# Optimization experiments

Hardware: AMD Instinct MI355X
Metric: run time of the kernel (lower is better)

## Reference

```python
import jax, jax.numpy as jnp
import numpy as np

B, S, H, F, E, K = 2, 2048, 1024, 4096, 8, 2
NH = H // 128  # heads of dim 128, per SimpleMoEBlock.__init__
DH = H // NH


def _layernorm(x, g, b, eps=1e-5):
    m = x.mean(-1, keepdims=True)
    v = ((x - m) ** 2).mean(-1, keepdims=True)
    return (x - m) / jnp.sqrt(v + eps) * g + b


def _forward(x, ln_attn_g, ln_attn_b, ln_mlp_g, ln_mlp_b,
             in_proj_w, in_proj_b, out_proj_w, out_proj_b,
             router_w, fc1_w, fc1_b, fc2_w, fc2_b):
    # --- self attention (nn.MultiheadAttention, batch_first, no mask) ---
    xa = _layernorm(x, ln_attn_g, ln_attn_b)                    # [B,S,H]
    qkv = xa @ in_proj_w.T + in_proj_b                          # [B,S,3H]
    q, k, v = jnp.split(qkv, 3, axis=-1)
    def heads(t):
        return t.reshape(B, S, NH, DH).transpose(0, 2, 1, 3)    # [B,NH,S,DH]
    q, k, v = heads(q), heads(k), heads(v)
    scores = jnp.einsum('bhqd,bhkd->bhqk', q, k) / jnp.sqrt(jnp.asarray(DH, x.dtype))
    attn = jnp.einsum('bhqk,bhkd->bhqd', jax.nn.softmax(scores, axis=-1), v)
    attn = attn.transpose(0, 2, 1, 3).reshape(B, S, H)
    attn = attn @ out_proj_w.T + out_proj_b
    h = x + attn                                                # residual

    # --- MoE feed-forward ---
    y = _layernorm(h, ln_mlp_g, ln_mlp_b).reshape(B * S, H)     # flat tokens [T,H]
    logits = y @ router_w.T                                     # [T,E]
    probs = jax.nn.softmax(logits, axis=-1)
    top_scores, top_idx = jax.lax.top_k(probs, K)               # [T,K]
    # per-token per-expert combine weight; 0 for unrouted tokens -> identical
    # math to torch's index_select/index_add dispatch
    w = (jax.nn.one_hot(top_idx, E, dtype=y.dtype) * top_scores[..., None]).sum(axis=1)  # [T,E]

    combined = jnp.zeros_like(y)
    for e in range(E):  # fixed small expert count
        he = jax.nn.silu(y @ fc1_w[e].T + fc1_b[e])             # [T,F]
        oe = he @ fc2_w[e].T + fc2_b[e]                         # [T,H]
        combined = combined + oe * w[:, e:e + 1]
    return h + combined.reshape(B, S, H)


def setup_inputs() -> dict:
    key = jax.random.key(0)
    ks = jax.random.split(key, 8)
    s = 0.02
    return {
        'x': jax.random.normal(ks[0], (B, S, H), jnp.float32),
        'ln_attn_g': jnp.ones((H,), jnp.float32),
        'ln_attn_b': jnp.zeros((H,), jnp.float32),
        'ln_mlp_g': jnp.ones((H,), jnp.float32),
        'ln_mlp_b': jnp.zeros((H,), jnp.float32),
        'in_proj_w': jax.random.normal(ks[1], (3 * H, H), jnp.float32) * s,
        'in_proj_b': jnp.zeros((3 * H,), jnp.float32),
        'out_proj_w': jax.random.normal(ks[2], (H, H), jnp.float32) * s,
        'out_proj_b': jnp.zeros((H,), jnp.float32),
        'router_w': jax.random.normal(ks[3], (E, H), jnp.float32) * s,
        'fc1_w': jax.random.normal(ks[4], (E, F, H), jnp.float32) * s,
        'fc1_b': jnp.zeros((E, F), jnp.float32),
        'fc2_w': jax.random.normal(ks[5], (E, H, F), jnp.float32) * s,
        'fc2_b': jnp.zeros((E, H), jnp.float32),
    }


def reference(x, ln_attn_g, ln_attn_b, ln_mlp_g, ln_mlp_b,
              in_proj_w, in_proj_b, out_proj_w, out_proj_b,
              router_w, fc1_w, fc1_b, fc2_w, fc2_b):
    return _forward(x, ln_attn_g, ln_attn_b, ln_mlp_g, ln_mlp_b,
                    in_proj_w, in_proj_b, out_proj_w, out_proj_b,
                    router_w, fc1_w, fc1_b, fc2_w, fc2_b)
```

## Files before the change

### kernel.cpp

```cpp
#include <hip/hip_runtime.h>

#define T_TOK 4096
#define S_SEQ 2048
#define H_DIM 1024
#define H3    3072
#define NHEAD 8
#define DHEAD 128
#define F_DIM 4096
#define NEXP  8
#define MAX_RB 72
#define NSLOT 9216

typedef __bf16 bf16x8 __attribute__((ext_vector_type(8)));
typedef float  f32x4  __attribute__((ext_vector_type(4)));
typedef __attribute__((address_space(1))) const unsigned int* gas1_t;
typedef __attribute__((address_space(3))) unsigned int* las3_t;

__device__ __forceinline__ unsigned short f2bf(float f){
  unsigned int u = __builtin_bit_cast(unsigned int, f);
  u += 0x7fffu + ((u>>16)&1u);
  return (unsigned short)(u>>16);
}
__device__ __forceinline__ float bf2f(unsigned short h){
  unsigned int u = ((unsigned int)h)<<16;
  return __builtin_bit_cast(float, u);
}
__device__ __forceinline__ f32x4 MF(bf16x8 a, bf16x8 b, f32x4 c){
  return __builtin_amdgcn_mfma_f32_16x16x32_bf16(a,b,c,0,0,0);
}
__device__ __forceinline__ void gload16(const void* g, void* l){
  __builtin_amdgcn_global_load_lds((gas1_t)g, (las3_t)l, 16, 0, 0);
}
__device__ __forceinline__ float blockReduceSum(float v){
  __shared__ float sh_red[4];
  #pragma unroll
  for(int o=32;o>0;o>>=1) v += __shfl_down(v,o,64);
  int w = threadIdx.x>>6;
  if((threadIdx.x&63)==0) sh_red[w]=v;
  __syncthreads();
  float tot = sh_red[0]+sh_red[1]+sh_red[2]+sh_red[3];
  __syncthreads();
  return tot;
}

__global__ __launch_bounds__(256) void k_ln_split(const float* __restrict__ x,
    const float* __restrict__ g, const float* __restrict__ bta,
    unsigned short* __restrict__ hi, unsigned short* __restrict__ lo){
  int t = blockIdx.x, tid = threadIdx.x;
  float4 v = reinterpret_cast<const float4*>(x + (size_t)t*H_DIM)[tid];
  float mean = blockReduceSum(v.x+v.y+v.z+v.w) * (1.0f/H_DIM);
  float d0=v.x-mean,d1=v.y-mean,d2=v.z-mean,d3=v.w-mean;
  float var = blockReduceSum(d0*d0+d1*d1+d2*d2+d3*d3) * (1.0f/H_DIM);
  float rstd = rsqrtf(var + 1e-5f);
  float4 gv = reinterpret_cast<const float4*>(g)[tid];
  float4 bv = reinterpret_cast<const float4*>(bta)[tid];
  float o0=d0*rstd*gv.x+bv.x, o1=d1*rstd*gv.y+bv.y, o2=d2*rstd*gv.z+bv.z, o3=d3*rstd*gv.w+bv.w;
  size_t base = (size_t)t*H_DIM + tid*4;
  unsigned short h0=f2bf(o0),h1=f2bf(o1),h2=f2bf(o2),h3=f2bf(o3);
  *reinterpret_cast<ushort4*>(hi+base) = make_ushort4(h0,h1,h2,h3);
  *reinterpret_cast<ushort4*>(lo+base) = make_ushort4(
      f2bf(o0-bf2f(h0)), f2bf(o1-bf2f(h1)), f2bf(o2-bf2f(h2)), f2bf(o3-bf2f(h3)));
}

__global__ __launch_bounds__(256) void k_wsplit(const float* __restrict__ w,
    unsigned short* __restrict__ hi, unsigned short* __restrict__ lo, int n4){
  int i = blockIdx.x*256 + threadIdx.x;
  if(i>=n4) return;
  float4 v = reinterpret_cast<const float4*>(w)[i];
  size_t base = (size_t)i*4;
  unsigned short h0=f2bf(v.x),h1=f2bf(v.y),h2=f2bf(v.z),h3=f2bf(v.w);
  *reinterpret_cast<ushort4*>(hi+base) = make_ushort4(h0,h1,h2,h3);
  *reinterpret_cast<ushort4*>(lo+base) = make_ushort4(
      f2bf(v.x-bf2f(h0)), f2bf(v.y-bf2f(h1)), f2bf(v.z-bf2f(h2)), f2bf(v.w-bf2f(h3)));
}

__global__ __launch_bounds__(256) void k_wconv(const float* __restrict__ w,
    unsigned short* __restrict__ hi, int n4){
  int i = blockIdx.x*256 + threadIdx.x;
  if(i>=n4) return;
  float4 v = reinterpret_cast<const float4*>(w)[i];
  *reinterpret_cast<ushort4*>(hi + (size_t)i*4) =
      make_ushort4(f2bf(v.x), f2bf(v.y), f2bf(v.z), f2bf(v.w));
}

template<int EPI>
__global__ __launch_bounds__(256) void k_gemm_split(
    const unsigned short* __restrict__ Ah, const unsigned short* __restrict__ Al,
    const unsigned short* __restrict__ Bh, const unsigned short* __restrict__ Bl,
    const float* __restrict__ bias, const float* __restrict__ resid,
    unsigned short* __restrict__ Chi, unsigned short* __restrict__ Clo,
    float* __restrict__ Cf, int N, int Kd){
  int m0 = blockIdx.y*128, n0 = blockIdx.x*128;
  int tid=threadIdx.x, wid=tid>>6, lane=tid&63, lr=lane&15, lg=lane>>4;
  int wr=wid>>1, wc=wid&1;
  __shared__ unsigned short tAh[4096], tAl[4096], tBh[4096], tBl[4096];
  f32x4 acc[4][4] = {};
  for(int k0=0;k0<Kd;k0+=32){
    #pragma unroll
    for(int i=0;i<2;i++){
      int p = i*256 + tid;
      int row = p>>2, pc = p&3;
      int lc = pc ^ ((row>>1)&3);
      size_t go = (size_t)row*Kd + k0 + lc*8;
      int lb = (i*256 + wid*64)*8;
      gload16(Ah + (size_t)m0*Kd + go, tAh + lb);
      gload16(Al + (size_t)m0*Kd + go, tAl + lb);
      gload16(Bh + (size_t)n0*Kd + go, tBh + lb);
      gload16(Bl + (size_t)n0*Kd + go, tBl + lb);
    }
    asm volatile("s_waitcnt vmcnt(0)" ::: "memory");
    __syncthreads();
    bf16x8 ah[4], al[4], bh[4], bl[4];
    #pragma unroll
    for(int q=0;q<4;q++){
      int ra = wr*64+q*16+lr;
      int ia = ra*32 + ((lg ^ ((ra>>1)&3))<<3);
      ah[q] = *reinterpret_cast<const bf16x8*>(&tAh[ia]);
      al[q] = *reinterpret_cast<const bf16x8*>(&tAl[ia]);
      int rb = wc*64+q*16+lr;
      int ib = rb*32 + ((lg ^ ((rb>>1)&3))<<3);
      bh[q] = *reinterpret_cast<const bf16x8*>(&tBh[ib]);
      bl[q] = *reinterpret_cast<const bf16x8*>(&tBl[ib]);
    }
    #pragma unroll
    for(int mf=0;mf<4;mf++)
      #pragma unroll
      for(int nf=0;nf<4;nf++){
        acc[mf][nf] = MF(ah[mf], bh[nf], acc[mf][nf]);
        acc[mf][nf] = MF(ah[mf], bl[nf], acc[mf][nf]);
        acc[mf][nf] = MF(al[mf], bh[nf], acc[mf][nf]);
      }
    __syncthreads();
  }
  #pragma unroll
  for(int mf=0;mf<4;mf++)
    #pragma unroll
    for(int nf=0;nf<4;nf++)
      #pragma unroll
      for(int r=0;r<4;r++){
        int row = m0 + wr*64 + mf*16 + lg*4 + r;
        int col = n0 + wc*64 + nf*16 + lr;
        float v = acc[mf][nf][r] + bias[col];
        size_t idx = (size_t)row*N + col;
        if(EPI==0){
          unsigned short hb = f2bf(v);
          Chi[idx]=hb; Clo[idx]=f2bf(v-bf2f(hb));
        } else {
          Cf[idx] = v + resid[idx];
        }
      }
}

__global__ __launch_bounds__(256) void k_vtrans(const unsigned short* __restrict__ qh,
    const unsigned short* __restrict__ ql,
    unsigned short* __restrict__ vth, unsigned short* __restrict__ vtl){
  int bh = blockIdx.z, d0 = blockIdx.y*32, s0 = blockIdx.x*32;
  int b = bh>>3, hh = bh&7;
  int tid=threadIdx.x;
  __shared__ unsigned short th[32][40], tl[32][40];
  int sr = tid>>3, dc = (tid&7)*4;
  size_t src = ((size_t)(b*S_SEQ + s0 + sr))*H3 + 2*H_DIM + hh*DHEAD + d0 + dc;
  *reinterpret_cast<ushort4*>(&th[sr][dc]) = *reinterpret_cast<const ushort4*>(qh+src);
  *reinterpret_cast<ushort4*>(&tl[sr][dc]) = *reinterpret_cast<const ushort4*>(ql+src);
  __syncthreads();
  int dr = tid>>3, sc = (tid&7)*4;
  size_t dst = ((size_t)(bh*DHEAD) + d0+dr)*S_SEQ + s0 + sc;
  *reinterpret_cast<ushort4*>(vth+dst) = make_ushort4(th[sc][dr],th[sc+1][dr],th[sc+2][dr],th[sc+3][dr]);
  *reinterpret_cast<ushort4*>(vtl+dst) = make_ushort4(tl[sc][dr],tl[sc+1][dr],tl[sc+2][dr],tl[sc+3][dr]);
}

__global__ __launch_bounds__(256) void k_attn(const unsigned short* __restrict__ qkv_hi,
    const unsigned short* __restrict__ qkv_lo,
    const unsigned short* __restrict__ vt_hi, const unsigned short* __restrict__ vt_lo,
    unsigned short* __restrict__ o_hi, unsigned short* __restrict__ o_lo){
  const float SCALE = 0.08838834764831843f;
  int qb = blockIdx.x, bh = blockIdx.y;
  int b = bh>>3, hh = bh&7;
  int tid=threadIdx.x, wid=tid>>6, lane=tid&63, lr=lane&15, lg=lane>>4;
  __shared__ unsigned short kh[4096], kl[4096], vh[4096], vl[4096];
  __shared__ unsigned short ph[4][512], pl[4][512];
  int qrow = qb*64 + wid*16 + lr;
  size_t qbase = ((size_t)(b*S_SEQ) + qrow)*H3 + hh*DHEAD;
  bf16x8 qh_[4], ql_[4];
  #pragma unroll
  for(int kk=0;kk<4;kk++){
    qh_[kk] = *reinterpret_cast<const bf16x8*>(qkv_hi + qbase + kk*32 + lg*8);
    ql_[kk] = *reinterpret_cast<const bf16x8*>(qkv_lo + qbase + kk*32 + lg*8);
  }
  f32x4 o_acc[8] = {};
  float mrun[4] = {-1e30f,-1e30f,-1e30f,-1e30f};
  float lrun[4] = {0.f,0.f,0.f,0.f};
  for(int kv0=0; kv0<S_SEQ; kv0+=32){
    #pragma unroll
    for(int i=0;i<2;i++){
      int p = i*256 + tid;
      {
        int row = p>>4, pc = p&15;
        int lc = (pc&8)|((pc&7)^(row&7));
        size_t go = ((size_t)(b*S_SEQ + kv0 + row))*H3 + H_DIM + hh*DHEAD + lc*8;
        int lb = (i*256 + wid*64)*8;
        gload16(qkv_hi + go, kh + lb);
        gload16(qkv_lo + go, kl + lb);
      }
      {
        int row = p>>2, pc = p&3;
        int lc = pc ^ ((row>>1)&3);
        size_t go = ((size_t)(bh*DHEAD) + row)*S_SEQ + kv0 + lc*8;
        int lb = (i*256 + wid*64)*8;
        gload16(vt_hi + go, vh + lb);
        gload16(vt_lo + go, vl + lb);
      }
    }
    asm volatile("s_waitcnt vmcnt(0)" ::: "memory");
    __syncthreads();
    f32x4 sa0 = {0.f,0.f,0.f,0.f}, sa1 = {0.f,0.f,0.f,0.f};
    #pragma unroll
    for(int kk=0;kk<4;kk++){
      int c = kk*4+lg;
      {
        int krow = lr;
        int idx = krow*128 + (((c&8)|((c&7)^(krow&7)))<<3);
        bf16x8 kb = *reinterpret_cast<const bf16x8*>(&kh[idx]);
        bf16x8 kc = *reinterpret_cast<const bf16x8*>(&kl[idx]);
        sa0 = MF(qh_[kk], kb, sa0); sa0 = MF(qh_[kk], kc, sa0); sa0 = MF(ql_[kk], kb, sa0);
      }
      {
        int krow = 16+lr;
        int idx = krow*128 + (((c&8)|((c&7)^(krow&7)))<<3);
        bf16x8 kb = *reinterpret_cast<const bf16x8*>(&kh[idx]);
        bf16x8 kc = *reinterpret_cast<const bf16x8*>(&kl[idx]);
        sa1 = MF(qh_[kk], kb, sa1); sa1 = MF(qh_[kk], kc, sa1); sa1 = MF(ql_[kk], kb, sa1);
      }
    }
    float resc[4];
    #pragma unroll
    for(int r=0;r<4;r++){
      float s0v = sa0[r]*SCALE, s1v = sa1[r]*SCALE;
      float m_ = fmaxf(s0v, s1v);
      #pragma unroll
      for(int off=1;off<16;off<<=1) m_ = fmaxf(m_, __shfl_xor(m_, off, 64));
      float mn = fmaxf(mrun[r], m_);
      float p0 = __expf(s0v - mn), p1 = __expf(s1v - mn);
      float ss = p0+p1;
      #pragma unroll
      for(int off=1;off<16;off<<=1) ss += __shfl_xor(ss, off, 64);
      resc[r] = __expf(mrun[r] - mn);
      lrun[r] = lrun[r]*resc[r] + ss;
      mrun[r] = mn;
      sa0[r] = p0; sa1[r] = p1;
    }
    #pragma unroll
    for(int nf2=0;nf2<8;nf2++){
      f32x4 t = o_acc[nf2];
      t[0]*=resc[0]; t[1]*=resc[1]; t[2]*=resc[2]; t[3]*=resc[3];
      o_acc[nf2] = t;
    }
    #pragma unroll
    for(int r=0;r<4;r++){
      int prow = lg*4 + r;
      int x0 = (prow>>1)&3;
      {
        int key = lr;
        int idx = prow*32 + (((key>>3)^x0)<<3) + (key&7);
        unsigned short hb = f2bf(sa0[r]);
        ph[wid][idx]=hb; pl[wid][idx]=f2bf(sa0[r]-bf2f(hb));
      }
      {
        int key = 16+lr;
        int idx = prow*32 + (((key>>3)^x0)<<3) + (key&7);
        unsigned short hb = f2bf(sa1[r]);
        ph[wid][idx]=hb; pl[wid][idx]=f2bf(sa1[r]-bf2f(hb));
      }
    }
    int physA = lg ^ ((lr>>1)&3);
    bf16x8 pah = *reinterpret_cast<const bf16x8*>(&ph[wid][lr*32 + physA*8]);
    bf16x8 pal = *reinterpret_cast<const bf16x8*>(&pl[wid][lr*32 + physA*8]);
    #pragma unroll
    for(int nf2=0;nf2<8;nf2++){
      int d = nf2*16 + lr;
      int idx = d*32 + ((lg ^ ((d>>1)&3))<<3);
      bf16x8 vb = *reinterpret_cast<const bf16x8*>(&vh[idx]);
      bf16x8 vc = *reinterpret_cast<const bf16x8*>(&vl[idx]);
      o_acc[nf2] = MF(pah, vb, o_acc[nf2]);
      o_acc[nf2] = MF(pah, vc, o_acc[nf2]);
      o_acc[nf2] = MF(pal, vb, o_acc[nf2]);
    }
    __syncthreads();
  }
  float linv[4];
  #pragma unroll
  for(int r=0;r<4;r++) linv[r] = 1.0f/lrun[r];
  #pragma unroll
  for(int nf2=0;nf2<8;nf2++)
    #pragma unroll
    for(int r=0;r<4;r++){
      float v = o_acc[nf2][r]*linv[r];
      int row = qb*64 + wid*16 + lg*4 + r;
      int col = hh*DHEAD + nf2*16 + lr;
      size_t idx = ((size_t)(b*S_SEQ + row))*H_DIM + col;
      unsigned short hb = f2bf(v);
      o_hi[idx]=hb; o_lo[idx]=f2bf(v - bf2f(hb));
    }
}

__global__ __launch_bounds__(256) void k_ln2_router(const float* __restrict__ h,
    const float* __restrict__ g, const float* __restrict__ bt, const float* __restrict__ rw,
    unsigned short* __restrict__ ybf, int* __restrict__ route_e, float* __restrict__ route_w){
  int t = blockIdx.x, tid = threadIdx.x;
  float4 v = reinterpret_cast<const float4*>(h + (size_t)t*H_DIM)[tid];
  float mean = blockReduceSum(v.x+v.y+v.z+v.w) * (1.0f/H_DIM);
  float d0=v.x-mean,d1=v.y-mean,d2=v.z-mean,d3=v.w-mean;
  float var = blockReduceSum(d0*d0+d1*d1+d2*d2+d3*d3) * (1.0f/H_DIM);
  float rstd = rsqrtf(var + 1e-5f);
  float4 gv = reinterpret_cast<const float4*>(g)[tid];
  float4 bv = reinterpret_cast<const float4*>(bt)[tid];
  float o0=d0*rstd*gv.x+bv.x, o1=d1*rstd*gv.y+bv.y, o2=d2*rstd*gv.z+bv.z, o3=d3*rstd*gv.w+bv.w;
  size_t base = (size_t)t*H_DIM + tid*4;
  *reinterpret_cast<ushort4*>(ybf+base) = make_ushort4(f2bf(o0),f2bf(o1),f2bf(o2),f2bf(o3));
  float part[8];
  #pragma unroll
  for(int e=0;e<8;e++){
    float4 r = reinterpret_cast<const float4*>(rw + e*H_DIM)[tid];
    part[e] = o0*r.x + o1*r.y + o2*r.z + o3*r.w;
  }
  __shared__ float sm[32];
  #pragma unroll
  for(int e=0;e<8;e++){
    float p = part[e];
    #pragma unroll
    for(int o=32;o>0;o>>=1) p += __shfl_down(p,o,64);
    if((tid&63)==0) sm[(tid>>6)*8+e] = p;
  }
  __syncthreads();
  if(tid==0){
    float lgt[8];
    #pragma unroll
    for(int e=0;e<8;e++) lgt[e] = sm[e]+sm[8+e]+sm[16+e]+sm[24+e];
    float mx = lgt[0];
    #pragma unroll
    for(int e=1;e<8;e++) mx = fmaxf(mx, lgt[e]);
    float ex[8], ssum=0.f;
    #pragma unroll
    for(int e=0;e<8;e++){ ex[e]=__expf(lgt[e]-mx); ssum+=ex[e]; }
    float inv = 1.0f/ssum;
    int e0=0; float p0=ex[0];
    for(int e=1;e<8;e++) if(ex[e]>p0){p0=ex[e];e0=e;}
    int e1=-1; float p1=-1.0f;
    for(int e=0;e<8;e++) if(e!=e0 && ex[e]>p1){p1=ex[e];e1=e;}
    route_e[2*t]=e0; route_e[2*t+1]=e1;
    route_w[2*t]=p0*inv; route_w[2*t+1]=p1*inv;
  }
}

__global__ __launch_bounds__(256) void k_compact(const int* __restrict__ route_e,
    const float* __restrict__ route_w, int* __restrict__ tok_of_slot,
    float* __restrict__ w_of_slot, int* __restrict__ slot_of_tok,
    int* __restrict__ rb_expert, int* __restrict__ rb_base){
  __shared__ int cnt[8], off[8], pos[8];
  int tid = threadIdx.x;
  if(tid<8){ cnt[tid]=0; pos[tid]=0; }
  __syncthreads();
  for(int t=tid;t<T_TOK;t+=256){
    atomicAdd(&cnt[route_e[2*t]],1);
    atomicAdd(&cnt[route_e[2*t+1]],1);
  }
  __syncthreads();
  if(tid==0){
    int o=0;
    for(int e=0;e<8;e++){ off[e]=o; o += ((cnt[e]+127)>>7)<<7; }
    int rb=0;
    for(int e=0;e<8;e++){
      int nrb = (cnt[e]+127)>>7;
      for(int r=0;r<nrb;r++){ rb_expert[rb]=e; rb_base[rb]=off[e]+r*128; rb++; }
    }
    for(;rb<MAX_RB;rb++){ rb_expert[rb]=-1; rb_base[rb]=0; }
  }
  __syncthreads();
  for(int s=tid;s<NSLOT;s+=256){ tok_of_slot[s]=0; w_of_slot[s]=0.0f; }
  __syncthreads();
  for(int t=tid;t<T_TOK;t+=256){
    int e0=route_e[2*t], e1=route_e[2*t+1];
    int s0 = off[e0] + atomicAdd(&pos[e0],1);
    tok_of_slot[s0]=t; w_of_slot[s0]=route_w[2*t]; slot_of_tok[2*t]=s0;
    int s1 = off[e1] + atomicAdd(&pos[e1],1);
    tok_of_slot[s1]=t; w_of_slot[s1]=route_w[2*t+1]; slot_of_tok[2*t+1]=s1;
  }
}

template<bool FC1, bool PRE>
__global__ __launch_bounds__(256) void k_fc(const unsigned short* __restrict__ Abuf,
    const float* __restrict__ W, const unsigned short* __restrict__ Wbf,
    const float* __restrict__ bias,
    const int* __restrict__ rb_expert, const int* __restrict__ rb_base,
    const int* __restrict__ tok_of_slot, const float* __restrict__ w_of_slot,
    unsigned short* __restrict__ he_out, float* __restrict__ oew_out){
  int rb = blockIdx.y;
  int e = rb_expert[rb];
  if(e<0) return;
  int base = rb_base[rb];
  int n0 = blockIdx.x*128;
  const int Kd = FC1 ? H_DIM : F_DIM;
  const int Nd = FC1 ? F_DIM : H_DIM;
  int tid=threadIdx.x, wid=tid>>6, lane=tid&63, lr=lane&15, lg=lane>>4;
  int wr=wid>>1, wc=wid&1;
  __shared__ unsigned short tA[4096], tB[4096];
  size_t arow_src[2];
  #pragma unroll
  for(int i=0;i<2;i++){
    int row = i*64 + (tid>>2);
    if(FC1){ int tok = tok_of_slot[base+row]; arow_src[i] = (size_t)tok*H_DIM; }
    else   { arow_src[i] = (size_t)(base+row)*F_DIM; }
  }
  const float* Wp = W + (size_t)e*F_DIM*H_DIM;
  const unsigned short* Wbp = Wbf + (size_t)e*F_DIM*H_DIM;
  f32x4 acc[4][4] = {};
  for(int k0=0;k0<Kd;k0+=32){
    #pragma unroll
    for(int i=0;i<2;i++){
      int p = i*256+tid; int row=p>>2, pc=p&3;
      int lc = pc ^ ((row>>1)&3);
      gload16(Abuf + arow_src[i] + k0 + lc*8, tA + (i*256+wid*64)*8);
      if(PRE){
        gload16(Wbp + (size_t)(n0+row)*Kd + k0 + lc*8, tB + (i*256+wid*64)*8);
      }
    }
    if(!PRE){
      #pragma unroll
      for(int j=0;j<4;j++){
        int f = tid*16 + j*4; int row=f>>5; int kin=f&31;
        float4 wv = *reinterpret_cast<const float4*>(Wp + (size_t)(n0+row)*Kd + k0 + kin);
        int c16 = kin>>3, half=(kin>>2)&1;
        int phys = c16 ^ ((row>>1)&3);
        *reinterpret_cast<ushort4*>(&tB[row*32 + phys*8 + half*4]) =
            make_ushort4(f2bf(wv.x), f2bf(wv.y), f2bf(wv.z), f2bf(wv.w));
      }
    }
    asm volatile("s_waitcnt vmcnt(0)" ::: "memory");
    __syncthreads();
    bf16x8 af[4], bfr[4];
    #pragma unroll
    for(int q=0;q<4;q++){
      int ra = wr*64+q*16+lr;
      af[q] = *reinterpret_cast<const bf16x8*>(&tA[ra*32 + ((lg ^ ((ra>>1)&3))<<3)]);
      int rbw = wc*64+q*16+lr;
      bfr[q] = *reinterpret_cast<const bf16x8*>(&tB[rbw*32 + ((lg ^ ((rbw>>1)&3))<<3)]);
    }
    #pragma unroll
    for(int mf=0;mf<4;mf++)
      #pragma unroll
      for(int nf=0;nf<4;nf++)
        acc[mf][nf] = MF(af[mf], bfr[nf], acc[mf][nf]);
    __syncthreads();
  }
  #pragma unroll
  for(int mf=0;mf<4;mf++)
    #pragma unroll
    for(int nf=0;nf<4;nf++)
      #pragma unroll
      for(int r=0;r<4;r++){
        int lrow = wr*64+mf*16+lg*4+r;
        int col = n0 + wc*64+nf*16+lr;
        float v = acc[mf][nf][r] + bias[(size_t)e*Nd + col];
        if(FC1){
          float sv = v/(1.0f+__expf(-v));
          he_out[(size_t)(base+lrow)*F_DIM + col] = f2bf(sv);
        } else {
          oew_out[(size_t)(base+lrow)*H_DIM + col] = w_of_slot[base+lrow]*v;
        }
      }
}

__global__ __launch_bounds__(256) void k_combine(const float* __restrict__ h,
    const float* __restrict__ oew, const int* __restrict__ slot_of_tok,
    float* __restrict__ out){
  int t = blockIdx.x, tid=threadIdx.x;
  int s0 = slot_of_tok[2*t], s1 = slot_of_tok[2*t+1];
  float4 hv = reinterpret_cast<const float4*>(h + (size_t)t*H_DIM)[tid];
  float4 a = reinterpret_cast<const float4*>(oew + (size_t)s0*H_DIM)[tid];
  float4 b = reinterpret_cast<const float4*>(oew + (size_t)s1*H_DIM)[tid];
  float4 o = make_float4(hv.x+a.x+b.x, hv.y+a.y+b.y, hv.z+a.z+b.z, hv.w+a.w+b.w);
  reinterpret_cast<float4*>(out + (size_t)t*H_DIM)[tid] = o;
}

extern "C" void kernel_launch(void* const* d_in, const int* in_sizes, int n_in,
                              void* d_out, int out_size, void* d_ws, size_t ws_size,
                              hipStream_t stream){
  const float* x    = (const float*)d_in[0];
  const float* ln1g = (const float*)d_in[1];
  const float* ln1b = (const float*)d_in[2];
  const float* ln2g = (const float*)d_in[3];
  const float* ln2b = (const float*)d_in[4];
  const float* wqkv = (const float*)d_in[5];
  const float* bqkv = (const float*)d_in[6];
  const float* wout = (const float*)d_in[7];
  const float* bout = (const float*)d_in[8];
  const float* rw   = (const float*)d_in[9];
  const float* fc1w = (const float*)d_in[10];
  const float* fc1b = (const float*)d_in[11];
  const float* fc2w = (const float*)d_in[12];
  const float* fc2b = (const float*)d_in[13];
  char* ws = (char*)d_ws;

  size_t off_ = 0;
  auto AL = [&](size_t bytes){ size_t r = off_; off_ = (off_ + bytes + 255) & ~(size_t)255; return r; };
  size_t o_xa_hi = AL((size_t)T_TOK*H_DIM*2), o_xa_lo = AL((size_t)T_TOK*H_DIM*2);
  size_t o_wq_hi = AL((size_t)H3*H_DIM*2),    o_wq_lo = AL((size_t)H3*H_DIM*2);
  size_t o_wo_hi = AL((size_t)H_DIM*H_DIM*2), o_wo_lo = AL((size_t)H_DIM*H_DIM*2);
  size_t o_qk_hi = AL((size_t)T_TOK*H3*2),    o_qk_lo = AL((size_t)T_TOK*H3*2);
  size_t o_vt_hi = AL((size_t)16*DHEAD*S_SEQ*2), o_vt_lo = AL((size_t)16*DHEAD*S_SEQ*2);
  size_t o_at_hi = AL((size_t)T_TOK*H_DIM*2), o_at_lo = AL((size_t)T_TOK*H_DIM*2);
  size_t o_he  = 0;
  size_t o_oew = (size_t)NSLOT*F_DIM*2;
  size_t o_h   = AL((size_t)T_TOK*H_DIM*4);
  size_t o_ybf = AL((size_t)T_TOK*H_DIM*2);
  size_t o_re  = AL((size_t)T_TOK*2*4);
  size_t o_rwt = AL((size_t)T_TOK*2*4);
  size_t o_st  = AL((size_t)T_TOK*2*4);
  size_t o_ts  = AL((size_t)NSLOT*4);
  size_t o_wsl = AL((size_t)NSLOT*4);
  size_t o_rbe = AL(4096);
  size_t o_rbb = AL(4096);
  size_t o_wb  = AL((size_t)NEXP*F_DIM*H_DIM*2);
  bool pre = (off_ <= ws_size);
  (void)in_sizes; (void)n_in; (void)out_size;

  unsigned short* xa_hi = (unsigned short*)(ws+o_xa_hi);
  unsigned short* xa_lo = (unsigned short*)(ws+o_xa_lo);
  unsigned short* wq_hi = (unsigned short*)(ws+o_wq_hi);
  unsigned short* wq_lo = (unsigned short*)(ws+o_wq_lo);
  unsigned short* wo_hi = (unsigned short*)(ws+o_wo_hi);
  unsigned short* wo_lo = (unsigned short*)(ws+o_wo_lo);
  unsigned short* qk_hi = (unsigned short*)(ws+o_qk_hi);
  unsigned short* qk_lo = (unsigned short*)(ws+o_qk_lo);
  unsigned short* vt_hi = (unsigned short*)(ws+o_vt_hi);
  unsigned short* vt_lo = (unsigned short*)(ws+o_vt_lo);
  unsigned short* at_hi = (unsigned short*)(ws+o_at_hi);
  unsigned short* at_lo = (unsigned short*)(ws+o_at_lo);
  unsigned short* he    = (unsigned short*)(ws+o_he);
  float* oew   = (float*)(ws+o_oew);
  float* hbuf  = (float*)(ws+o_h);
  unsigned short* ybf = (unsigned short*)(ws+o_ybf);
  int*   route_e = (int*)(ws+o_re);
  float* route_w = (float*)(ws+o_rwt);
  int*   slot_of_tok = (int*)(ws+o_st);
  int*   tok_of_slot = (int*)(ws+o_ts);
  float* w_of_slot   = (float*)(ws+o_wsl);
  int*   rb_expert   = (int*)(ws+o_rbe);
  int*   rb_base     = (int*)(ws+o_rbb);
  unsigned short* wb = (unsigned short*)(ws+o_wb);

  k_ln_split<<<T_TOK, 256, 0, stream>>>(x, ln1g, ln1b, xa_hi, xa_lo);
  k_wsplit<<<(H3*H_DIM/4+255)/256, 256, 0, stream>>>(wqkv, wq_hi, wq_lo, H3*H_DIM/4);
  k_wsplit<<<(H_DIM*H_DIM/4+255)/256, 256, 0, stream>>>(wout, wo_hi, wo_lo, H_DIM*H_DIM/4);
  k_gemm_split<0><<<dim3(H3/128, T_TOK/128), 256, 0, stream>>>(
      xa_hi, xa_lo, wq_hi, wq_lo, bqkv, nullptr, qk_hi, qk_lo, nullptr, H3, H_DIM);
  k_vtrans<<<dim3(S_SEQ/32, DHEAD/32, 16), 256, 0, stream>>>(qk_hi, qk_lo, vt_hi, vt_lo);
  k_attn<<<dim3(S_SEQ/64, 16), 256, 0, stream>>>(qk_hi, qk_lo, vt_hi, vt_lo, at_hi, at_lo);
  k_gemm_split<1><<<dim3(H_DIM/128, T_TOK/128), 256, 0, stream>>>(
      at_hi, at_lo, wo_hi, wo_lo, bout, x, nullptr, nullptr, hbuf, H_DIM, H_DIM);
  k_ln2_router<<<T_TOK, 256, 0, stream>>>(hbuf, ln2g, ln2b, rw, ybf, route_e, route_w);
  k_compact<<<1, 256, 0, stream>>>(route_e, route_w, tok_of_slot, w_of_slot,
                                   slot_of_tok, rb_expert, rb_base);
  const int WN4 = NEXP*F_DIM*H_DIM/4;
  if(pre){
    k_wconv<<<(WN4+255)/256, 256, 0, stream>>>(fc1w, wb, WN4);
    k_fc<true,true><<<dim3(F_DIM/128, MAX_RB), 256, 0, stream>>>(
        ybf, fc1w, wb, fc1b, rb_expert, rb_base, tok_of_slot, nullptr, he, nullptr);
    k_wconv<<<(WN4+255)/256, 256, 0, stream>>>(fc2w, wb, WN4);
    k_fc<false,true><<<dim3(H_DIM/128, MAX_RB), 256, 0, stream>>>(
        he, fc2w, wb, fc2b, rb_expert, rb_base, tok_of_slot, w_of_slot, nullptr, oew);
  } else {
    k_fc<true,false><<<dim3(F_DIM/128, MAX_RB), 256, 0, stream>>>(
        ybf, fc1w, wb, fc1b, rb_expert, rb_base, tok_of_slot, nullptr, he, nullptr);
    k_fc<false,false><<<dim3(H_DIM/128, MAX_RB), 256, 0, stream>>>(
        he, fc2w, wb, fc2b, rb_expert, rb_base, tok_of_slot, w_of_slot, nullptr, oew);
  }
  k_combine<<<T_TOK, 256, 0, stream>>>(hbuf, oew, slot_of_tok, (float*)d_out);
}
```

Measured before the change: 733.8 us.

## Restructure attention kernel: double-buffered KV, 128-row Q tiles, transposed MFMA, lazy rescale

Rewrites the flash attention kernel. K/V tiles are now double-buffered so the next tile's global loads overlap the current tile's compute, and each wave covers 32 query rows, so every K/V tile loaded into LDS is reused across more queries. The MFMA operands are swapped so scores come out transposed, which turns the row reductions into two cross-lane shuffles and allows vectorized P and output stores. The output rescale is skipped while the new max stays within 8 of the running max. The costs are doubled LDS, more registers (launch bounds min 1 block), and half as many blocks, which lowers occupancy and parallelism.

```diff
diff --git a/kernel.cpp b/kernel.cpp
--- a/kernel.cpp
+++ b/kernel.cpp
@@ -169,7 +169,7 @@
   *reinterpret_cast<ushort4*>(vtl+dst) = make_ushort4(tl[sc][dr],tl[sc+1][dr],tl[sc+2][dr],tl[sc+3][dr]);
 }
 
-__global__ __launch_bounds__(256) void k_attn(const unsigned short* __restrict__ qkv_hi,
+__global__ __launch_bounds__(256,1) void k_attn(const unsigned short* __restrict__ qkv_hi,
     const unsigned short* __restrict__ qkv_lo,
     const unsigned short* __restrict__ vt_hi, const unsigned short* __restrict__ vt_lo,
     unsigned short* __restrict__ o_hi, unsigned short* __restrict__ o_lo){
@@ -177,130 +177,156 @@
   int qb = blockIdx.x, bh = blockIdx.y;
   int b = bh>>3, hh = bh&7;
   int tid=threadIdx.x, wid=tid>>6, lane=tid&63, lr=lane&15, lg=lane>>4;
-  __shared__ unsigned short kh[4096], kl[4096], vh[4096], vl[4096];
-  __shared__ unsigned short ph[4][512], pl[4][512];
-  int qrow = qb*64 + wid*16 + lr;
-  size_t qbase = ((size_t)(b*S_SEQ) + qrow)*H3 + hh*DHEAD;
-  bf16x8 qh_[4], ql_[4];
-  #pragma unroll
-  for(int kk=0;kk<4;kk++){
-    qh_[kk] = *reinterpret_cast<const bf16x8*>(qkv_hi + qbase + kk*32 + lg*8);
-    ql_[kk] = *reinterpret_cast<const bf16x8*>(qkv_lo + qbase + kk*32 + lg*8);
-  }
-  f32x4 o_acc[8] = {};
-  float mrun[4] = {-1e30f,-1e30f,-1e30f,-1e30f};
-  float lrun[4] = {0.f,0.f,0.f,0.f};
-  for(int kv0=0; kv0<S_SEQ; kv0+=32){
+  __shared__ unsigned short kh[2][4096], kl[2][4096], vh[2][4096], vl[2][4096];
+  __shared__ unsigned short ph[4][1024], pl[4][1024];
+  int row0 = qb*128 + wid*32;
+  bf16x8 qh_[2][4], ql_[2][4];
+  #pragma unroll
+  for(int j=0;j<2;j++){
+    size_t qbase = ((size_t)(b*S_SEQ) + row0 + j*16 + lr)*H3 + hh*DHEAD;
+    #pragma unroll
+    for(int kk=0;kk<4;kk++){
+      qh_[j][kk] = *reinterpret_cast<const bf16x8*>(qkv_hi + qbase + kk*32 + lg*8);
+      ql_[j][kk] = *reinterpret_cast<const bf16x8*>(qkv_lo + qbase + kk*32 + lg*8);
+    }
+  }
+  f32x4 o_acc[2][8] = {};
+  float mrun[2] = {-1e30f,-1e30f};
+  float lrun[2] = {0.f,0.f};
+
+  auto STAGE = [&](int buf, int kv0){
     #pragma unroll
     for(int i=0;i<2;i++){
       int p = i*256 + tid;
+      int lb = (i*256 + wid*64)*8;
       {
-        int row = p>>4, pc = p&15;
-        int lc = (pc&8)|((pc&7)^(row&7));
-        size_t go = ((size_t)(b*S_SEQ + kv0 + row))*H3 + H_DIM + hh*DHEAD + lc*8;
-        int lb = (i*256 + wid*64)*8;
-        gload16(qkv_hi + go, kh + lb);
-        gload16(qkv_lo + go, kl + lb);
+        int krow = p>>4, pc = p&15;
+        int lc = (pc&8)|((pc&7)^(krow&7));
+        size_t go = ((size_t)(b*S_SEQ + kv0 + krow))*H3 + H_DIM + hh*DHEAD + lc*8;
+        gload16(qkv_hi + go, &kh[buf][lb]);
+        gload16(qkv_lo + go, &kl[buf][lb]);
       }
       {
-        int row = p>>2, pc = p&3;
-        int lc = pc ^ ((row>>1)&3);
-        size_t go = ((size_t)(bh*DHEAD) + row)*S_SEQ + kv0 + lc*8;
-        int lb = (i*256 + wid*64)*8;
-        gload16(vt_hi + go, vh + lb);
-        gload16(vt_lo + go, vl + lb);
+        int vrow = p>>2, pc = p&3;
+        int lc = pc ^ ((vrow>>1)&3);
+        size_t gv = ((size_t)(bh*DHEAD) + vrow)*S_SEQ + kv0 + lc*8;
+        gload16(vt_hi + gv, &vh[buf][lb]);
+        gload16(vt_lo + gv, &vl[buf][lb]);
+      }
+    }
+  };
+
+  STAGE(0, 0);
+  asm volatile("s_waitcnt vmcnt(0)" ::: "memory");
+  __syncthreads();
+  int cur = 0;
+  for(int kv0=0; kv0<S_SEQ; kv0+=32){
+    if(kv0+32 < S_SEQ) STAGE(cur^1, kv0+32);
+    f32x4 s0[2] = {}, s1[2] = {};
+    #pragma unroll
+    for(int kk=0;kk<4;kk++){
+      int c = kk*4+lg;
+      int phys = (c&8)|((c&7)^(lr&7));
+      bf16x8 kah = *reinterpret_cast<const bf16x8*>(&kh[cur][lr*128 + phys*8]);
+      bf16x8 kal = *reinterpret_cast<const bf16x8*>(&kl[cur][lr*128 + phys*8]);
+      bf16x8 kbh = *reinterpret_cast<const bf16x8*>(&kh[cur][(16+lr)*128 + phys*8]);
+      bf16x8 kbl = *reinterpret_cast<const bf16x8*>(&kl[cur][(16+lr)*128 + phys*8]);
+      #pragma unroll
+      for(int j=0;j<2;j++){
+        s0[j] = MF(kah, qh_[j][kk], s0[j]);
+        s0[j] = MF(kah, ql_[j][kk], s0[j]);
+        s0[j] = MF(kal, qh_[j][kk], s0[j]);
+        s1[j] = MF(kbh, qh_[j][kk], s1[j]);
+        s1[j] = MF(kbh, ql_[j][kk], s1[j]);
+        s1[j] = MF(kbl, qh_[j][kk], s1[j]);
+      }
+    }
+    float sc[2][8]; float mt[2];
+    #pragma unroll
+    for(int j=0;j<2;j++){
+      #pragma unroll
+      for(int r=0;r<4;r++){ sc[j][r] = s0[j][r]*SCALE; sc[j][4+r] = s1[j][r]*SCALE; }
+      float m_ = fmaxf(fmaxf(fmaxf(sc[j][0],sc[j][1]),fmaxf(sc[j][2],sc[j][3])),
+                       fmaxf(fmaxf(sc[j][4],sc[j][5]),fmaxf(sc[j][6],sc[j][7])));
+      m_ = fmaxf(m_, __shfl_xor(m_,16,64));
+      m_ = fmaxf(m_, __shfl_xor(m_,32,64));
+      mt[j] = m_;
+    }
+    int skip = __all((mt[0] <= mrun[0]+8.0f) && (mt[1] <= mrun[1]+8.0f));
+    if(!skip){
+      #pragma unroll
+      for(int j=0;j<2;j++){
+        float mn = fmaxf(mrun[j], mt[j]);
+        float rs = __expf(mrun[j]-mn);
+        lrun[j] *= rs; mrun[j] = mn;
+        #pragma unroll
+        for(int nf2=0;nf2<8;nf2++){
+          f32x4 t = o_acc[j][nf2];
+          t[0]*=rs; t[1]*=rs; t[2]*=rs; t[3]*=rs;
+          o_acc[j][nf2] = t;
+        }
+      }
+    }
+    #pragma unroll
+    for(int j=0;j<2;j++){
+      float ssum = 0.f;
+      #pragma unroll
+      for(int i=0;i<8;i++){ sc[j][i] = __expf(sc[j][i]-mrun[j]); ssum += sc[j][i]; }
+      ssum += __shfl_xor(ssum,16,64);
+      ssum += __shfl_xor(ssum,32,64);
+      lrun[j] += ssum;
+      unsigned short hbk[8], lbk[8];
+      #pragma unroll
+      for(int i=0;i<8;i++){ hbk[i]=f2bf(sc[j][i]); lbk[i]=f2bf(sc[j][i]-bf2f(hbk[i])); }
+      int half = (lg&1)*4;
+      int a0 = j*512 + lr*32 + (((lg>>1)^(lr&3))<<3) + half;
+      int a1 = j*512 + lr*32 + ((((lg>>1)+2)^(lr&3))<<3) + half;
+      *reinterpret_cast<ushort4*>(&ph[wid][a0]) = make_ushort4(hbk[0],hbk[1],hbk[2],hbk[3]);
+      *reinterpret_cast<ushort4*>(&pl[wid][a0]) = make_ushort4(lbk[0],lbk[1],lbk[2],lbk[3]);
+      *reinterpret_cast<ushort4*>(&ph[wid][a1]) = make_ushort4(hbk[4],hbk[5],hbk[6],hbk[7]);
+      *reinterpret_cast<ushort4*>(&pl[wid][a1]) = make_ushort4(lbk[4],lbk[5],lbk[6],lbk[7]);
+    }
+    bf16x8 pbh[2], pbl[2];
+    #pragma unroll
+    for(int j=0;j<2;j++){
+      int pp = (lg^(lr&3))<<3;
+      pbh[j] = *reinterpret_cast<const bf16x8*>(&ph[wid][j*512 + lr*32 + pp]);
+      pbl[j] = *reinterpret_cast<const bf16x8*>(&pl[wid][j*512 + lr*32 + pp]);
+    }
+    #pragma unroll
+    for(int nf2=0;nf2<8;nf2++){
+      int d = nf2*16 + lr;
+      int vp = (lg ^ ((lr>>1)&3))<<3;
+      bf16x8 vah = *reinterpret_cast<const bf16x8*>(&vh[cur][d*32 + vp]);
+      bf16x8 val = *reinterpret_cast<const bf16x8*>(&vl[cur][d*32 + vp]);
+      #pragma unroll
+      for(int j=0;j<2;j++){
+        o_acc[j][nf2] = MF(vah, pbh[j], o_acc[j][nf2]);
+        o_acc[j][nf2] = MF(vah, pbl[j], o_acc[j][nf2]);
+        o_acc[j][nf2] = MF(val, pbh[j], o_acc[j][nf2]);
       }
     }
     asm volatile("s_waitcnt vmcnt(0)" ::: "memory");
     __syncthreads();
-    f32x4 sa0 = {0.f,0.f,0.f,0.f}, sa1 = {0.f,0.f,0.f,0.f};
-    #pragma unroll
-    for(int kk=0;kk<4;kk++){
-      int c = kk*4+lg;
-      {
-        int krow = lr;
-        int idx = krow*128 + (((c&8)|((c&7)^(krow&7)))<<3);
-        bf16x8 kb = *reinterpret_cast<const bf16x8*>(&kh[idx]);
-        bf16x8 kc = *reinterpret_cast<const bf16x8*>(&kl[idx]);
-        sa0 = MF(qh_[kk], kb, sa0); sa0 = MF(qh_[kk], kc, sa0); sa0 = MF(ql_[kk], kb, sa0);
-      }
-      {
-        int krow = 16+lr;
-        int idx = krow*128 + (((c&8)|((c&7)^(krow&7)))<<3);
-        bf16x8 kb = *reinterpret_cast<const bf16x8*>(&kh[idx]);
-        bf16x8 kc = *reinterpret_cast<const bf16x8*>(&kl[idx]);
-        sa1 = MF(qh_[kk], kb, sa1); sa1 = MF(qh_[kk], kc, sa1); sa1 = MF(ql_[kk], kb, sa1);
-      }
-    }
-    float resc[4];
-    #pragma unroll
-    for(int r=0;r<4;r++){
-      float s0v = sa0[r]*SCALE, s1v = sa1[r]*SCALE;
-      float m_ = fmaxf(s0v, s1v);
-      #pragma unroll
-      for(int off=1;off<16;off<<=1) m_ = fmaxf(m_, __shfl_xor(m_, off, 64));
-      float mn = fmaxf(mrun[r], m_);
-      float p0 = __expf(s0v - mn), p1 = __expf(s1v - mn);
-      float ss = p0+p1;
-      #pragma unroll
-      for(int off=1;off<16;off<<=1) ss += __shfl_xor(ss, off, 64);
-      resc[r] = __expf(mrun[r] - mn);
-      lrun[r] = lrun[r]*resc[r] + ss;
-      mrun[r] = mn;
-      sa0[r] = p0; sa1[r] = p1;
-    }
+    cur ^= 1;
+  }
+  #pragma unroll
+  for(int j=0;j<2;j++){
+    float linv = 1.0f/lrun[j];
+    size_t rowg = (size_t)(b*S_SEQ + row0 + j*16 + lr);
     #pragma unroll
     for(int nf2=0;nf2<8;nf2++){
-      f32x4 t = o_acc[nf2];
-      t[0]*=resc[0]; t[1]*=resc[1]; t[2]*=resc[2]; t[3]*=resc[3];
-      o_acc[nf2] = t;
-    }
-    #pragma unroll
-    for(int r=0;r<4;r++){
-      int prow = lg*4 + r;
-      int x0 = (prow>>1)&3;
-      {
-        int key = lr;
-        int idx = prow*32 + (((key>>3)^x0)<<3) + (key&7);
-        unsigned short hb = f2bf(sa0[r]);
-        ph[wid][idx]=hb; pl[wid][idx]=f2bf(sa0[r]-bf2f(hb));
-      }
-      {
-        int key = 16+lr;
-        int idx = prow*32 + (((key>>3)^x0)<<3) + (key&7);
-        unsigned short hb = f2bf(sa1[r]);
-        ph[wid][idx]=hb; pl[wid][idx]=f2bf(sa1[r]-bf2f(hb));
-      }
-    }
-    int physA = lg ^ ((lr>>1)&3);
-    bf16x8 pah = *reinterpret_cast<const bf16x8*>(&ph[wid][lr*32 + physA*8]);
-    bf16x8 pal = *reinterpret_cast<const bf16x8*>(&pl[wid][lr*32 + physA*8]);
-    #pragma unroll
-    for(int nf2=0;nf2<8;nf2++){
-      int d = nf2*16 + lr;
-      int idx = d*32 + ((lg ^ ((d>>1)&3))<<3);
-      bf16x8 vb = *reinterpret_cast<const bf16x8*>(&vh[idx]);
-      bf16x8 vc = *reinterpret_cast<const bf16x8*>(&vl[idx]);
-      o_acc[nf2] = MF(pah, vb, o_acc[nf2]);
-      o_acc[nf2] = MF(pah, vc, o_acc[nf2]);
-      o_acc[nf2] = MF(pal, vb, o_acc[nf2]);
-    }
-    __syncthreads();
-  }
-  float linv[4];
-  #pragma unroll
-  for(int r=0;r<4;r++) linv[r] = 1.0f/lrun[r];
-  #pragma unroll
-  for(int nf2=0;nf2<8;nf2++)
-    #pragma unroll
-    for(int r=0;r<4;r++){
-      float v = o_acc[nf2][r]*linv[r];
-      int row = qb*64 + wid*16 + lg*4 + r;
-      int col = hh*DHEAD + nf2*16 + lr;
-      size_t idx = ((size_t)(b*S_SEQ + row))*H_DIM + col;
-      unsigned short hb = f2bf(v);
-      o_hi[idx]=hb; o_lo[idx]=f2bf(v - bf2f(hb));
-    }
+      unsigned short hp[4], lp[4];
+      #pragma unroll
+      for(int r=0;r<4;r++){
+        float v = o_acc[j][nf2][r]*linv;
+        hp[r] = f2bf(v); lp[r] = f2bf(v - bf2f(hp[r]));
+      }
+      size_t idx = rowg*H_DIM + hh*DHEAD + nf2*16 + lg*4;
+      *reinterpret_cast<ushort4*>(o_hi+idx) = make_ushort4(hp[0],hp[1],hp[2],hp[3]);
+      *reinterpret_cast<ushort4*>(o_lo+idx) = make_ushort4(lp[0],lp[1],lp[2],lp[3]);
+    }
+  }
 }
 
 __global__ __launch_bounds__(256) void k_ln2_router(const float* __restrict__ h,
@@ -555,7 +581,7 @@
   k_gemm_split<0><<<dim3(H3/128, T_TOK/128), 256, 0, stream>>>(
       xa_hi, xa_lo, wq_hi, wq_lo, bqkv, nullptr, qk_hi, qk_lo, nullptr, H3, H_DIM);
   k_vtrans<<<dim3(S_SEQ/32, DHEAD/32, 16), 256, 0, stream>>>(qk_hi, qk_lo, vt_hi, vt_lo);
-  k_attn<<<dim3(S_SEQ/64, 16), 256, 0, stream>>>(qk_hi, qk_lo, vt_hi, vt_lo, at_hi, at_lo);
+  k_attn<<<dim3(S_SEQ/128, 16), 256, 0, stream>>>(qk_hi, qk_lo, vt_hi, vt_lo, at_hi, at_lo);
   k_gemm_split<1><<<dim3(H_DIM/128, T_TOK/128), 256, 0, stream>>>(
       at_hi, at_lo, wo_hi, wo_lo, bout, x, nullptr, nullptr, hbuf, H_DIM, H_DIM);
   k_ln2_router<<<T_TOK, 256, 0, stream>>>(hbuf, ln2g, ln2b, rw, ybf, route_e, route_w);
```

New measurement: 725.4 us. About the same (-1.2%).
